# Kernel tuning notes

Measured on AMD Instinct MI355X. Metric: run time of the kernel, lower is better.

## Reference

```python
import jax, jax.numpy as jnp
import numpy as np

H = 8  # hidden_size


def lstm_layer(x, w_ih, w_hh, b_ih, b_hh):
    """Single LSTM layer, seq-first x: [T, B, in] -> hidden seq [T, B, H].
    PyTorch gate order: i, f, g, o."""
    # Precompute input contribution for all timesteps (one big GEMM).
    zx = jnp.einsum('tbi,gi->tbg', x, w_ih) + b_ih + b_hh  # [T, B, 4H]
    B = x.shape[1]
    h0 = jnp.zeros((B, H), x.dtype)
    c0 = jnp.zeros((B, H), x.dtype)

    def step(carry, zx_t):
        h, c = carry
        z = zx_t + h @ w_hh.T  # [B, 4H]
        i = jax.nn.sigmoid(z[:, 0 * H:1 * H])
        f = jax.nn.sigmoid(z[:, 1 * H:2 * H])
        g = jnp.tanh(z[:, 2 * H:3 * H])
        o = jax.nn.sigmoid(z[:, 3 * H:4 * H])
        c_new = f * c + i * g
        h_new = o * jnp.tanh(c_new)
        return (h_new, c_new), h_new

    _, hs = jax.lax.scan(step, (h0, c0), zx)
    return hs  # [T, B, H]


def setup_inputs() -> dict:
    key = jax.random.key(0)
    ks = jax.random.split(key, 12)
    T, B, IN, OUT = 1024, 16384, 2, 1
    k = 1.0 / np.sqrt(H)  # torch default init bound

    def unif(kk, shape):
        return jax.random.uniform(kk, shape, jnp.float32, -k, k)

    x = jax.random.normal(ks[0], (T, B, IN), jnp.float32)
    return {
        'x': x,
        'w_ih_l0': unif(ks[1], (4 * H, IN)),
        'w_hh_l0': unif(ks[2], (4 * H, H)),
        'b_ih_l0': unif(ks[3], (4 * H,)),
        'b_hh_l0': unif(ks[4], (4 * H,)),
        'w_ih_l1': unif(ks[5], (4 * H, H)),
        'w_hh_l1': unif(ks[6], (4 * H, H)),
        'b_ih_l1': unif(ks[7], (4 * H,)),
        'b_hh_l1': unif(ks[8], (4 * H,)),
        'fc_w': unif(ks[9], (OUT, H)),
        'fc_b': unif(ks[10], (OUT,)),
    }


def reference(x, w_ih_l0, w_hh_l0, b_ih_l0, b_hh_l0,
              w_ih_l1, w_hh_l1, b_ih_l1, b_hh_l1, fc_w, fc_b):
    h = lstm_layer(x, w_ih_l0, w_hh_l0, b_ih_l0, b_hh_l0)   # layer 0
    h = lstm_layer(h, w_ih_l1, w_hh_l1, b_ih_l1, b_hh_l1)   # layer 1
    last = h[-1]                                            # [B, H]
    return last @ fc_w.T + fc_b                             # [B, out]
```

## Files before the change

### kernel.cpp

```cpp
#include <hip/hip_runtime.h>

#define TSTEPS 1024
#define BATCH 16384

typedef float f32x2 __attribute__((ext_vector_type(2)));

template<int K>
__device__ __forceinline__ float bc8(float v) {
    return __int_as_float(__builtin_amdgcn_ds_swizzle(__float_as_int(v), (K << 5) | 0x18));
}
__device__ __forceinline__ void gather8(float* d, float v) {
    d[0] = bc8<0>(v); d[1] = bc8<1>(v); d[2] = bc8<2>(v); d[3] = bc8<3>(v);
    d[4] = bc8<4>(v); d[5] = bc8<5>(v); d[6] = bc8<6>(v); d[7] = bc8<7>(v);
}

__device__ __forceinline__ f32x2 fma2(f32x2 a, f32x2 b, f32x2 c) {
    return __builtin_elementwise_fma(a, b, c);
}
__device__ __forceinline__ f32x2 splat2(float v) { f32x2 r; r.x = v; r.y = v; return r; }

__device__ __forceinline__ float sig_s(float zs) {
    return __builtin_amdgcn_rcpf(1.0f + __builtin_amdgcn_exp2f(zs));
}
__device__ __forceinline__ float tanh_s(float zs) {
    return __builtin_fmaf(2.0f, __builtin_amdgcn_rcpf(1.0f + __builtin_amdgcn_exp2f(zs)), -1.0f);
}
__device__ __forceinline__ float tanh_raw(float c) { return tanh_s(c * -2.88539008f); }

__global__ __launch_bounds__(256, 2) void lstm2_fused(
    const float* __restrict__ x,
    const float* __restrict__ w_ih_l0, const float* __restrict__ w_hh_l0,
    const float* __restrict__ b_ih_l0, const float* __restrict__ b_hh_l0,
    const float* __restrict__ w_ih_l1, const float* __restrict__ w_hh_l1,
    const float* __restrict__ b_ih_l1, const float* __restrict__ b_hh_l1,
    const float* __restrict__ fc_w, const float* __restrict__ fc_b,
    float* __restrict__ out)
{
    const int tid = blockIdx.x * blockDim.x + threadIdx.x;
    const int j = tid & 7;
    const int b = tid >> 3;

    const float sc[4] = {-1.44269504f, -1.44269504f, -2.88539008f, -1.44269504f};

    f32x2 wi0xp[2], wi0yp[2], zb0p[2], zb1p[2];
    f32x2 wh0p[2][8], wi1p[2][8], wh1p[2][8];
#pragma unroll
    for (int p = 0; p < 2; ++p) {
        const int ga = 2 * p, gb = 2 * p + 1;
        const int ra = ga * 8 + j, rb = gb * 8 + j;
        const float sa = sc[ga], sb = sc[gb];
        wi0xp[p].x = sa * w_ih_l0[ra * 2 + 0]; wi0xp[p].y = sb * w_ih_l0[rb * 2 + 0];
        wi0yp[p].x = sa * w_ih_l0[ra * 2 + 1]; wi0yp[p].y = sb * w_ih_l0[rb * 2 + 1];
        zb0p[p].x = sa * (b_ih_l0[ra] + b_hh_l0[ra]);
        zb0p[p].y = sb * (b_ih_l0[rb] + b_hh_l0[rb]);
        zb1p[p].x = sa * (b_ih_l1[ra] + b_hh_l1[ra]);
        zb1p[p].y = sb * (b_ih_l1[rb] + b_hh_l1[rb]);
#pragma unroll
        for (int k = 0; k < 8; ++k) {
            wh0p[p][k].x = sa * w_hh_l0[ra * 8 + k]; wh0p[p][k].y = sb * w_hh_l0[rb * 8 + k];
            wi1p[p][k].x = sa * w_ih_l1[ra * 8 + k]; wi1p[p][k].y = sb * w_ih_l1[rb * 8 + k];
            wh1p[p][k].x = sa * w_hh_l1[ra * 8 + k]; wh1p[p][k].y = sb * w_hh_l1[rb * 8 + k];
        }
    }
#pragma unroll
    for (int p = 0; p < 2; ++p) {
        asm volatile("" : "+v"(wi0xp[p]), "+v"(wi0yp[p]), "+v"(zb0p[p]), "+v"(zb1p[p]));
#pragma unroll
        for (int k = 0; k < 8; ++k)
            asm volatile("" : "+v"(wh0p[p][k]), "+v"(wi1p[p][k]), "+v"(wh1p[p][k]));
    }
    const float fcw = fc_w[j];
    const float fcb = fc_b[0];

    float h0 = 0.f, c0 = 0.f, h1 = 0.f, c1 = 0.f;
    float h0v[8], h1v[8];
#pragma unroll
    for (int k = 0; k < 8; ++k) { h0v[k] = 0.f; h1v[k] = 0.f; }

    const float2* xp = reinterpret_cast<const float2*>(x) + b;
    float2 xv = xp[0];
    float2 xn = xp[BATCH];

    for (int t = 0; t < TSTEPS; ++t) {
        float2 xn2 = (t + 2 < TSTEPS) ? xp[2 * BATCH] : xv;
        xp += BATCH;

        f32x2 z0[2], z1[2];
#pragma unroll
        for (int p = 0; p < 2; ++p) {
            z0[p] = fma2(wi0yp[p], splat2(xv.y), fma2(wi0xp[p], splat2(xv.x), zb0p[p]));
            z1[p] = zb1p[p];
#pragma unroll
            for (int k = 0; k < 8; ++k) {
                z0[p] = fma2(wh0p[p][k], splat2(h0v[k]), z0[p]);
                z1[p] = fma2(wh1p[p][k], splat2(h1v[k]), z1[p]);
            }
        }
        const float gi = sig_s(z0[0].x), gf = sig_s(z0[0].y);
        const float gg = tanh_s(z0[1].x), go = sig_s(z0[1].y);
        c0 = __builtin_fmaf(gf, c0, gi * gg);
        h0 = go * tanh_raw(c0);

        gather8(h0v, h0);
#pragma unroll
        for (int p = 0; p < 2; ++p)
#pragma unroll
            for (int k = 0; k < 8; ++k)
                z1[p] = fma2(wi1p[p][k], splat2(h0v[k]), z1[p]);

        const float i1 = sig_s(z1[0].x), f1 = sig_s(z1[0].y);
        const float g1 = tanh_s(z1[1].x), o1 = sig_s(z1[1].y);
        c1 = __builtin_fmaf(f1, c1, i1 * g1);
        h1 = o1 * tanh_raw(c1);

        gather8(h1v, h1);

        xv = xn; xn = xn2;
    }

    float p = fcw * h1;
    p += __shfl_xor(p, 1);
    p += __shfl_xor(p, 2);
    p += __shfl_xor(p, 4);
    if (j == 0) out[b] = p + fcb;
}

extern "C" void kernel_launch(void* const* d_in, const int* in_sizes, int n_in,
                              void* d_out, int out_size, void* d_ws, size_t ws_size,
                              hipStream_t stream) {
    const float* x       = (const float*)d_in[0];
    const float* w_ih_l0 = (const float*)d_in[1];
    const float* w_hh_l0 = (const float*)d_in[2];
    const float* b_ih_l0 = (const float*)d_in[3];
    const float* b_hh_l0 = (const float*)d_in[4];
    const float* w_ih_l1 = (const float*)d_in[5];
    const float* w_hh_l1 = (const float*)d_in[6];
    const float* b_ih_l1 = (const float*)d_in[7];
    const float* b_hh_l1 = (const float*)d_in[8];
    const float* fc_w    = (const float*)d_in[9];
    const float* fc_b    = (const float*)d_in[10];
    float* out = (float*)d_out;

    const int threads = 256;
    const int blocks  = (BATCH * 8) / threads;
    lstm2_fused<<<blocks, threads, 0, stream>>>(
        x, w_ih_l0, w_hh_l0, b_ih_l0, b_hh_l0,
        w_ih_l1, w_hh_l1, b_ih_l1, b_hh_l1, fc_w, fc_b, out);
}
```

Baseline: 927.5 us.

## Split each LSTM row across 16 lanes with cross-lane reduction of gate sums

Each batch element is now handled by 16 lanes instead of 8, with each half computing partial gate pre-activations over half of the hidden inputs (and one of the two input features). Partial sums are combined via a swizzle xor-8 add, and hidden-state broadcasts use ds_bpermute. This halves per-thread FMA work and register use, allowing more resident waves per SIMD for latency hiding. In exchange it adds reduction steps to the serial per-timestep critical path and duplicates activation math across halves.

After: 1.121 ms. 1.21x slower.

```diff
diff --git a/kernel.cpp b/kernel.cpp
--- a/kernel.cpp
+++ b/kernel.cpp
@@ -9,11 +9,15 @@
 __device__ __forceinline__ float bc8(float v) {
     return __int_as_float(__builtin_amdgcn_ds_swizzle(__float_as_int(v), (K << 5) | 0x18));
 }
-__device__ __forceinline__ void gather8(float* d, float v) {
-    d[0] = bc8<0>(v); d[1] = bc8<1>(v); d[2] = bc8<2>(v); d[3] = bc8<3>(v);
-    d[4] = bc8<4>(v); d[5] = bc8<5>(v); d[6] = bc8<6>(v); d[7] = bc8<7>(v);
+__device__ __forceinline__ float swz_xor8(float v) {
+    return __int_as_float(__builtin_amdgcn_ds_swizzle(__float_as_int(v), 0x201F));
 }
-
+__device__ __forceinline__ f32x2 swz_xor8_2(f32x2 v) {
+    f32x2 r; r.x = swz_xor8(v.x); r.y = swz_xor8(v.y); return r;
+}
+__device__ __forceinline__ float bperm(int addr, float v) {
+    return __int_as_float(__builtin_amdgcn_ds_bpermute(addr, __float_as_int(v)));
+}
 __device__ __forceinline__ f32x2 fma2(f32x2 a, f32x2 b, f32x2 c) {
     return __builtin_elementwise_fma(a, b, c);
 }
@@ -27,7 +31,7 @@
 }
 __device__ __forceinline__ float tanh_raw(float c) { return tanh_s(c * -2.88539008f); }
 
-__global__ __launch_bounds__(256, 2) void lstm2_fused(
+__global__ __launch_bounds__(256, 4) void lstm2_fused(
     const float* __restrict__ x,
     const float* __restrict__ w_ih_l0, const float* __restrict__ w_hh_l0,
     const float* __restrict__ b_ih_l0, const float* __restrict__ b_hh_l0,
@@ -36,93 +40,110 @@
     const float* __restrict__ fc_w, const float* __restrict__ fc_b,
     float* __restrict__ out)
 {
-    const int tid = blockIdx.x * blockDim.x + threadIdx.x;
-    const int j = tid & 7;
-    const int b = tid >> 3;
+    const int tid  = blockIdx.x * blockDim.x + threadIdx.x;
+    const int j    = tid & 7;
+    const int half = (tid >> 3) & 1;
+    const int b    = tid >> 4;
+    const int lane = threadIdx.x & 63;
 
     const float sc[4] = {-1.44269504f, -1.44269504f, -2.88539008f, -1.44269504f};
 
-    f32x2 wi0xp[2], wi0yp[2], zb0p[2], zb1p[2];
-    f32x2 wh0p[2][8], wi1p[2][8], wh1p[2][8];
+    f32x2 wi0a[2], zb0p[2], zb1p[2];
+    f32x2 wh0p[2][4], wi1p[2][4], wh1p[2][4];
 #pragma unroll
     for (int p = 0; p < 2; ++p) {
         const int ga = 2 * p, gb = 2 * p + 1;
         const int ra = ga * 8 + j, rb = gb * 8 + j;
         const float sa = sc[ga], sb = sc[gb];
-        wi0xp[p].x = sa * w_ih_l0[ra * 2 + 0]; wi0xp[p].y = sb * w_ih_l0[rb * 2 + 0];
-        wi0yp[p].x = sa * w_ih_l0[ra * 2 + 1]; wi0yp[p].y = sb * w_ih_l0[rb * 2 + 1];
-        zb0p[p].x = sa * (b_ih_l0[ra] + b_hh_l0[ra]);
-        zb0p[p].y = sb * (b_ih_l0[rb] + b_hh_l0[rb]);
-        zb1p[p].x = sa * (b_ih_l1[ra] + b_hh_l1[ra]);
-        zb1p[p].y = sb * (b_ih_l1[rb] + b_hh_l1[rb]);
+        wi0a[p].x = sa * w_ih_l0[ra * 2 + half];
+        wi0a[p].y = sb * w_ih_l0[rb * 2 + half];
+        zb0p[p].x = half ? 0.f : sa * (b_ih_l0[ra] + b_hh_l0[ra]);
+        zb0p[p].y = half ? 0.f : sb * (b_ih_l0[rb] + b_hh_l0[rb]);
+        zb1p[p].x = half ? 0.f : sa * (b_ih_l1[ra] + b_hh_l1[ra]);
+        zb1p[p].y = half ? 0.f : sb * (b_ih_l1[rb] + b_hh_l1[rb]);
 #pragma unroll
-        for (int k = 0; k < 8; ++k) {
-            wh0p[p][k].x = sa * w_hh_l0[ra * 8 + k]; wh0p[p][k].y = sb * w_hh_l0[rb * 8 + k];
-            wi1p[p][k].x = sa * w_ih_l1[ra * 8 + k]; wi1p[p][k].y = sb * w_ih_l1[rb * 8 + k];
-            wh1p[p][k].x = sa * w_hh_l1[ra * 8 + k]; wh1p[p][k].y = sb * w_hh_l1[rb * 8 + k];
+        for (int kp = 0; kp < 4; ++kp) {
+            const int k = half * 4 + kp;
+            wh0p[p][kp].x = sa * w_hh_l0[ra * 8 + k]; wh0p[p][kp].y = sb * w_hh_l0[rb * 8 + k];
+            wi1p[p][kp].x = sa * w_ih_l1[ra * 8 + k]; wi1p[p][kp].y = sb * w_ih_l1[rb * 8 + k];
+            wh1p[p][kp].x = sa * w_hh_l1[ra * 8 + k]; wh1p[p][kp].y = sb * w_hh_l1[rb * 8 + k];
         }
     }
 #pragma unroll
     for (int p = 0; p < 2; ++p) {
-        asm volatile("" : "+v"(wi0xp[p]), "+v"(wi0yp[p]), "+v"(zb0p[p]), "+v"(zb1p[p]));
+        asm volatile("" : "+v"(wi0a[p]), "+v"(zb0p[p]), "+v"(zb1p[p]));
 #pragma unroll
-        for (int k = 0; k < 8; ++k)
-            asm volatile("" : "+v"(wh0p[p][k]), "+v"(wi1p[p][k]), "+v"(wh1p[p][k]));
+        for (int kp = 0; kp < 4; ++kp)
+            asm volatile("" : "+v"(wh0p[p][kp]), "+v"(wi1p[p][kp]), "+v"(wh1p[p][kp]));
     }
+
+    int bpa[4];
+#pragma unroll
+    for (int kp = 0; kp < 4; ++kp) bpa[kp] = ((lane & 0x38) | (half * 4 + kp)) << 2;
+
     const float fcw = fc_w[j];
     const float fcb = fc_b[0];
 
     float h0 = 0.f, c0 = 0.f, h1 = 0.f, c1 = 0.f;
-    float h0v[8], h1v[8];
+    float h0v[4], h1v[4];
 #pragma unroll
-    for (int k = 0; k < 8; ++k) { h0v[k] = 0.f; h1v[k] = 0.f; }
+    for (int kp = 0; kp < 4; ++kp) { h0v[kp] = 0.f; h1v[kp] = 0.f; }
 
-    const float2* xp = reinterpret_cast<const float2*>(x) + b;
-    float2 xv = xp[0];
-    float2 xn = xp[BATCH];
+    const float* xp = x + b * 2 + half;
+    float xs = xp[0];
+    float xn = xp[2 * BATCH];
 
     for (int t = 0; t < TSTEPS; ++t) {
-        float2 xn2 = (t + 2 < TSTEPS) ? xp[2 * BATCH] : xv;
-        xp += BATCH;
+        float xn2 = (t + 2 < TSTEPS) ? xp[4 * BATCH] : xs;
+        xp += 2 * BATCH;
 
-        f32x2 z0[2], z1[2];
+        f32x2 z0p[2], z1p[2];
 #pragma unroll
         for (int p = 0; p < 2; ++p) {
-            z0[p] = fma2(wi0yp[p], splat2(xv.y), fma2(wi0xp[p], splat2(xv.x), zb0p[p]));
-            z1[p] = zb1p[p];
+            z0p[p] = fma2(wi0a[p], splat2(xs), zb0p[p]);
+            z1p[p] = zb1p[p];
 #pragma unroll
-            for (int k = 0; k < 8; ++k) {
-                z0[p] = fma2(wh0p[p][k], splat2(h0v[k]), z0[p]);
-                z1[p] = fma2(wh1p[p][k], splat2(h1v[k]), z1[p]);
+            for (int kp = 0; kp < 4; ++kp) {
+                z0p[p] = fma2(wh0p[p][kp], splat2(h0v[kp]), z0p[p]);
+                z1p[p] = fma2(wh1p[p][kp], splat2(h1v[kp]), z1p[p]);
             }
         }
-        const float gi = sig_s(z0[0].x), gf = sig_s(z0[0].y);
-        const float gg = tanh_s(z0[1].x), go = sig_s(z0[1].y);
+#pragma unroll
+        for (int p = 0; p < 2; ++p) z0p[p] = z0p[p] + swz_xor8_2(z0p[p]);
+
+        const float gi = sig_s(z0p[0].x), gf = sig_s(z0p[0].y);
+        const float gg = tanh_s(z0p[1].x), go = sig_s(z0p[1].y);
         c0 = __builtin_fmaf(gf, c0, gi * gg);
         h0 = go * tanh_raw(c0);
 
-        gather8(h0v, h0);
+#pragma unroll
+        for (int kp = 0; kp < 4; ++kp) h0v[kp] = bperm(bpa[kp], h0);
+
 #pragma unroll
         for (int p = 0; p < 2; ++p)
 #pragma unroll
-            for (int k = 0; k < 8; ++k)
-                z1[p] = fma2(wi1p[p][k], splat2(h0v[k]), z1[p]);
+            for (int kp = 0; kp < 4; ++kp)
+                z1p[p] = fma2(wi1p[p][kp], splat2(h0v[kp]), z1p[p]);
 
-        const float i1 = sig_s(z1[0].x), f1 = sig_s(z1[0].y);
-        const float g1 = tanh_s(z1[1].x), o1 = sig_s(z1[1].y);
+#pragma unroll
+        for (int p = 0; p < 2; ++p) z1p[p] = z1p[p] + swz_xor8_2(z1p[p]);
+
+        const float i1 = sig_s(z1p[0].x), f1 = sig_s(z1p[0].y);
+        const float g1 = tanh_s(z1p[1].x), o1 = sig_s(z1p[1].y);
         c1 = __builtin_fmaf(f1, c1, i1 * g1);
         h1 = o1 * tanh_raw(c1);
 
-        gather8(h1v, h1);
+#pragma unroll
+        for (int kp = 0; kp < 4; ++kp) h1v[kp] = bperm(bpa[kp], h1);
 
-        xv = xn; xn = xn2;
+        xs = xn; xn = xn2;
     }
 
     float p = fcw * h1;
     p += __shfl_xor(p, 1);
     p += __shfl_xor(p, 2);
     p += __shfl_xor(p, 4);
-    if (j == 0) out[b] = p + fcb;
+    if ((tid & 15) == 0) out[b] = p + fcb;
 }
 
 extern "C" void kernel_launch(void* const* d_in, const int* in_sizes, int n_in,
@@ -142,7 +163,7 @@
     float* out = (float*)d_out;
 
     const int threads = 256;
-    const int blocks  = (BATCH * 8) / threads;
+    const int blocks  = (BATCH * 16) / threads;
     lstm2_fused<<<blocks, threads, 0, stream>>>(
         x, w_ih_l0, w_hh_l0, b_ih_l0, b_hh_l0,
         w_ih_l1, w_hh_l1, b_ih_l1, b_hh_l1, fc_w, fc_b, out);
```
